# Kernel tuning notes

Hardware: AMD Instinct MI355X
Metric: run time of the kernel (lower is better)

Reference implementation:

```python
import jax, jax.numpy as jnp
import numpy as np

NF4 = jnp.array([-1.0, -0.6961928009986877, -0.5250730514526367, -0.39491748809814453,
                 -0.28444138169288635, -0.18477343022823334, -0.09105003625154495, 0.0,
                 0.07958029955625534, 0.16093020141124725, 0.24611230850219726,
                 0.33791524171829224, 0.44070982933044434, 0.5626170039176941,
                 0.7229568362236023, 1.0], dtype=jnp.float32)

OUT, IN = 8192, 8192
BLOCK = 64
NUMEL = OUT * IN


def setup_inputs() -> dict:
    key = jax.random.key(0)
    k1, k2, k3, k4 = jax.random.split(key, 4)
    x = jax.random.normal(k1, (64, IN), dtype=jnp.float32)
    packed = jax.random.randint(k2, (NUMEL // 2,), 0, 256, dtype=jnp.int32)
    absmax = jax.random.uniform(k3, (NUMEL // BLOCK,), dtype=jnp.float32)
    bias = jax.random.normal(k4, (OUT,), dtype=jnp.float32)
    return {"x": x, "packed": packed, "absmax": absmax, "bias": bias}


def nf4_dequantize(packed, absmax):
    # packed holds two 4-bit codes per byte: low nibble first, then high nibble
    low = packed & 15
    high = (packed >> 4) & 15
    q = jnp.stack([low, high], axis=1).reshape(-1)          # [numel]
    normalized = NF4[q]                                      # LUT dequant
    groups = normalized.reshape(-1, BLOCK)                   # [numel/block, block]
    w = (groups * absmax[:, None]).reshape(-1)[:NUMEL]
    return w.reshape(OUT, IN)


def reference(x, packed, absmax, bias):
    w = nf4_dequantize(packed, absmax)                       # [out, in]
    return jnp.dot(x, w.T) + bias                            # F.linear
```

## Files before the change

### kernel.cpp

```cpp
#include <hip/hip_runtime.h>
#include <hip/hip_bf16.h>

#define OUT_N 8192
#define IN_K  8192
#define M_ROWS 64

typedef __attribute__((ext_vector_type(8))) short  bf16x8;
typedef __attribute__((ext_vector_type(4))) float  f32x4;
typedef __attribute__((ext_vector_type(4))) int    int4v;

__device__ const float NF4_TAB[16] = {
  -1.0f, -0.6961928009986877f, -0.5250730514526367f, -0.39491748809814453f,
  -0.28444138169288635f, -0.18477343022823334f, -0.09105003625154495f, 0.0f,
  0.07958029955625534f, 0.16093020141124725f, 0.24611230850219726f,
  0.33791524171829224f, 0.44070982933044434f, 0.5626170039176941f,
  0.7229568362236023f, 1.0f };

static __device__ __forceinline__ unsigned short f2bf(float f) {
  union { __hip_bfloat16 h; unsigned short s; } u;
  u.h = __float2bfloat16(f);
  return u.s;
}

static __device__ __forceinline__ void gload_lds16(const void* g, void* s) {
  __builtin_amdgcn_global_load_lds((const __attribute__((address_space(1))) void*)g,
                                   (__attribute__((address_space(3))) void*)s,
                                   16, 0, 0);
}

__global__ __launch_bounds__(256) void qlin_prep(const float* __restrict__ x,
                                                 unsigned short* __restrict__ xf) {
  int t = blockIdx.x * 256 + threadIdx.x;
  int lane = t & 63, mt = (t >> 6) & 3, ks = t >> 8;
  int ri = lane & 15, kbb = lane >> 4;
  const float* src = x + (size_t)(mt * 16 + ri) * IN_K + ks * 32 + kbb * 8;
  f32x4 a = *(const f32x4*)src;
  f32x4 c = *(const f32x4*)(src + 4);
  bf16x8 o;
  o[0] = (short)f2bf(a[0]); o[1] = (short)f2bf(a[1]);
  o[2] = (short)f2bf(a[2]); o[3] = (short)f2bf(a[3]);
  o[4] = (short)f2bf(c[0]); o[5] = (short)f2bf(c[1]);
  o[6] = (short)f2bf(c[2]); o[7] = (short)f2bf(c[3]);
  ((bf16x8*)xf)[t] = o;
}

static __device__ __forceinline__ bf16x8 deq(const unsigned int* lut, int4v cur) {
  int4v bw;
  bw[0] = (int)lut[cur[0] & 255];
  bw[1] = (int)lut[cur[1] & 255];
  bw[2] = (int)lut[cur[2] & 255];
  bw[3] = (int)lut[cur[3] & 255];
  union { int4v i; bf16x8 h; } c; c.i = bw;
  return c.h;
}

#define STAGE(BUF, PH) {                                                      \
    const char* _s = xfb + (((size_t)(PH) * 4 + w) * 4096) + l * 16;          \
    gload_lds16(_s,        &ast[BUF][w][0]);                                  \
    gload_lds16(_s + 1024, &ast[BUF][w][64]);                                 \
    gload_lds16(_s + 2048, &ast[BUF][w][128]);                                \
    gload_lds16(_s + 3072, &ast[BUF][w][192]); }

#define CSTEP_BODY(S, PKV)                                                    \
    int _nk = KS + (S) + 4; if (_nk > NITm1) _nk = NITm1;                     \
    int4v _npk = *(const int4v*)(pcoal + (size_t)_nk * 64);                   \
    bf16x8 A0 = ast[cur][S][l];                                               \
    bf16x8 A1 = ast[cur][S][64 + l];                                          \
    bf16x8 A2 = ast[cur][S][128 + l];                                         \
    bf16x8 A3 = ast[cur][S][192 + l];                                         \
    int4v _c;                                                                 \
    _c[0] = __builtin_amdgcn_ds_bpermute(bpidx, PKV[0]);                      \
    _c[1] = __builtin_amdgcn_ds_bpermute(bpidx, PKV[1]);                      \
    _c[2] = __builtin_amdgcn_ds_bpermute(bpidx, PKV[2]);                      \
    _c[3] = __builtin_amdgcn_ds_bpermute(bpidx, PKV[3]);                      \
    bf16x8 b = deq(lut, _c);

#define CSTEP_EVEN(S, PKV) {                                                  \
    CSTEP_BODY(S, PKV)                                                        \
    sb0 = __builtin_amdgcn_mfma_f32_16x16x32_bf16(A0, b, zro, 0, 0, 0);       \
    sb1 = __builtin_amdgcn_mfma_f32_16x16x32_bf16(A1, b, zro, 0, 0, 0);       \
    sb2 = __builtin_amdgcn_mfma_f32_16x16x32_bf16(A2, b, zro, 0, 0, 0);       \
    sb3 = __builtin_amdgcn_mfma_f32_16x16x32_bf16(A3, b, zro, 0, 0, 0);       \
    PKV = _npk; }

#define CSTEP_ODD(S, PKV, AM) {                                               \
    CSTEP_BODY(S, PKV)                                                        \
    sb0 = __builtin_amdgcn_mfma_f32_16x16x32_bf16(A0, b, sb0, 0, 0, 0);       \
    sb1 = __builtin_amdgcn_mfma_f32_16x16x32_bf16(A1, b, sb1, 0, 0, 0);       \
    sb2 = __builtin_amdgcn_mfma_f32_16x16x32_bf16(A2, b, sb2, 0, 0, 0);       \
    sb3 = __builtin_amdgcn_mfma_f32_16x16x32_bf16(A3, b, sb3, 0, 0, 0);       \
    mn0 += sb0 * (AM); mn1 += sb1 * (AM);                                     \
    mn2 += sb2 * (AM); mn3 += sb3 * (AM);                                     \
    PKV = _npk; }

template<int NC>
__global__ __launch_bounds__(256, 4) void qlin_main(
    const int*   __restrict__ packed,
    const float* __restrict__ absmax,
    const unsigned short* __restrict__ xf,
    float*       __restrict__ parts) {
  constexpr int KCn   = IN_K / NC;
  constexpr int NIT   = KCn / 32;
  constexpr int NITm1 = NIT - 1;
  constexpr int NPH   = NIT / 4;
  constexpr int AMX   = NIT / 2 - 1;
  constexpr int LOG   = (NC == 8) ? 3 : 2;

  __shared__ unsigned int lut[256];
  __shared__ bf16x8 ast[2][4][256];
  {
    int t = threadIdx.x;
    unsigned lo = f2bf(NF4_TAB[t & 15]);
    unsigned hi = f2bf(NF4_TAB[(t >> 4) & 15]);
    lut[t] = lo | (hi << 16);
  }
  __syncthreads();

  const int l     = threadIdx.x & 63;
  const int w     = threadIdx.x >> 6;
  const int ntile = (int)blockIdx.x >> LOG;
  const int chunk = (int)blockIdx.x & (NC - 1);
  const int colg0 = ntile * 64 + w * 16;
  const int col   = colg0 + (l & 15);
  const int kb    = l >> 4;
  const int kc0   = chunk * KCn;
  const int ksg0  = kc0 >> 5;

  const char* pcoal = (const char*)packed
                    + ((size_t)(colg0 + (l >> 2)) * (IN_K / 2) + kc0 / 2) * 4
                    + (l & 3) * 16;
  const int bpidx = (((l & 15) << 2) | (l >> 4)) << 2;

  const char* xfb = (const char*)xf + (size_t)ksg0 * 4096;
  const float* aptr = absmax + (size_t)col * 128 + (kc0 >> 6);

  const f32x4 zro = {0.f, 0.f, 0.f, 0.f};
  f32x4 mn0 = zro, mn1 = zro, mn2 = zro, mn3 = zro;
  f32x4 sb0, sb1, sb2, sb3;
  int4v pk0, pk1, pk2, pk3;

  float amE = aptr[0], amO = aptr[1];
  STAGE(0, 0);
  __builtin_amdgcn_sched_barrier(0);
  pk0 = *(const int4v*)(pcoal);
  pk1 = *(const int4v*)(pcoal + 64);
  pk2 = *(const int4v*)(pcoal + 128);
  pk3 = *(const int4v*)(pcoal + 192);
  asm volatile("s_waitcnt vmcnt(4)" ::: "memory");
  __builtin_amdgcn_s_barrier();

  for (int ph = 0; ph < NPH; ++ph) {
    const int KS  = ph * 4;
    const int cur = ph & 1;

    int ia = 2 * ph + 2; if (ia > AMX) ia = AMX;
    int ib = 2 * ph + 3; if (ib > AMX) ib = AMX;
    float pmE = aptr[ia], pmO = aptr[ib];
    if (ph + 1 < NPH) STAGE(cur ^ 1, ph + 1);
    __builtin_amdgcn_sched_barrier(0);

    CSTEP_EVEN(0, pk0)
    CSTEP_ODD (1, pk1, amE)
    CSTEP_EVEN(2, pk2)
    CSTEP_ODD (3, pk3, amO)

    amE = pmE; amO = pmO;
    asm volatile("s_waitcnt vmcnt(4)" ::: "memory");
    asm volatile("s_waitcnt lgkmcnt(0)" ::: "memory");
    __builtin_amdgcn_s_barrier();
  }

  {
    float* tl = (float*)&ast[0][0][0];
    const int c  = w * 16 + (l & 15);
    const int r0 = kb * 4;
    tl[(0  + r0 + 0) * 68 + c] = mn0[0];
    tl[(0  + r0 + 1) * 68 + c] = mn0[1];
    tl[(0  + r0 + 2) * 68 + c] = mn0[2];
    tl[(0  + r0 + 3) * 68 + c] = mn0[3];
    tl[(16 + r0 + 0) * 68 + c] = mn1[0];
    tl[(16 + r0 + 1) * 68 + c] = mn1[1];
    tl[(16 + r0 + 2) * 68 + c] = mn1[2];
    tl[(16 + r0 + 3) * 68 + c] = mn1[3];
    tl[(32 + r0 + 0) * 68 + c] = mn2[0];
    tl[(32 + r0 + 1) * 68 + c] = mn2[1];
    tl[(32 + r0 + 2) * 68 + c] = mn2[2];
    tl[(32 + r0 + 3) * 68 + c] = mn2[3];
    tl[(48 + r0 + 0) * 68 + c] = mn3[0];
    tl[(48 + r0 + 1) * 68 + c] = mn3[1];
    tl[(48 + r0 + 2) * 68 + c] = mn3[2];
    tl[(48 + r0 + 3) * 68 + c] = mn3[3];
    __syncthreads();
    float* po = parts + (size_t)chunk * M_ROWS * OUT_N + (size_t)ntile * 64;
    const int t  = threadIdx.x;
    const int rr = t >> 4;
    const int cq = (t & 15) * 4;
    #pragma unroll
    for (int p = 0; p < 4; ++p) {
      const int row = p * 16 + rr;
      f32x4 v = *(const f32x4*)&tl[row * 68 + cq];
      *(f32x4*)(po + (size_t)row * OUT_N + cq) = v;
    }
  }
}

template<int NC>
__global__ __launch_bounds__(256) void qlin_reduce(
    const float* __restrict__ parts,
    const float* __restrict__ bias,
    float*       __restrict__ out) {
  const int TOT4 = M_ROWS * OUT_N / 4;
  int i4 = blockIdx.x * 256 + threadIdx.x;
  if (i4 >= TOT4) return;
  const f32x4* p = (const f32x4*)parts;
  f32x4 s = p[i4];
  #pragma unroll
  for (int c = 1; c < NC; ++c) s += p[i4 + c * TOT4];
  f32x4 bb = ((const f32x4*)bias)[i4 & (OUT_N / 4 - 1)];
  ((f32x4*)out)[i4] = s + bb;
}

extern "C" void kernel_launch(void* const* d_in, const int* in_sizes, int n_in,
                              void* d_out, int out_size, void* d_ws, size_t ws_size,
                              hipStream_t stream) {
  const float* x      = (const float*)d_in[0];
  const int*   packed = (const int*)d_in[1];
  const float* absmax = (const float*)d_in[2];
  const float* bias   = (const float*)d_in[3];
  float* out = (float*)d_out;

  unsigned short* xf = (unsigned short*)d_ws;
  float* parts = (float*)((char*)d_ws + (1 << 20));

  qlin_prep<<<(M_ROWS * IN_K / 8 + 255) / 256, 256, 0, stream>>>(x, xf);

  const size_t need8 = (size_t)(1 << 20)
                     + (size_t)8 * M_ROWS * OUT_N * sizeof(float);
  if (ws_size >= need8) {
    qlin_main<8><<<(OUT_N / 64) * 8, 256, 0, stream>>>(packed, absmax, xf, parts);
    qlin_reduce<8><<<(M_ROWS * OUT_N / 4 + 255) / 256, 256, 0, stream>>>(parts, bias, out);
  } else {
    qlin_main<4><<<(OUT_N / 64) * 4, 256, 0, stream>>>(packed, absmax, xf, parts);
    qlin_reduce<4><<<(M_ROWS * OUT_N / 4 + 255) / 256, 256, 0, stream>>>(parts, bias, out);
  }
}
```

Baseline: 41.61 us.

## Store split-K partials as bf16 tiles and pack bytes before a single bpermute

The split-K partial sums are now written as bf16 in a tile-contiguous layout, and the reduce kernel reads 8 bf16 per thread and accumulates in fp32. This halves partial-sum write and read traffic, at the cost of bf16 rounding error in each partial. Separately, the four packed bytes per step are combined into one 32-bit word, so one ds_bpermute is issued instead of four, which lowers cross-lane shuffle work in the inner loop. This assumes PKV elements hold values in 0..255, which holds when packed bytes are stored as int32.

After: 38.83 us, median of 2. -6.7%, faster.

```diff
diff --git a/kernel.cpp b/kernel.cpp
--- a/kernel.cpp
+++ b/kernel.cpp
@@ -8,6 +8,7 @@
 typedef __attribute__((ext_vector_type(8))) short  bf16x8;
 typedef __attribute__((ext_vector_type(4))) float  f32x4;
 typedef __attribute__((ext_vector_type(4))) int    int4v;
+typedef __attribute__((ext_vector_type(2))) int    int2v;
 
 __device__ const float NF4_TAB[16] = {
   -1.0f, -0.6961928009986877f, -0.5250730514526367f, -0.39491748809814453f,
@@ -44,12 +45,12 @@
   ((bf16x8*)xf)[t] = o;
 }
 
-static __device__ __forceinline__ bf16x8 deq(const unsigned int* lut, int4v cur) {
+static __device__ __forceinline__ bf16x8 deq(const unsigned int* lut, unsigned b) {
   int4v bw;
-  bw[0] = (int)lut[cur[0] & 255];
-  bw[1] = (int)lut[cur[1] & 255];
-  bw[2] = (int)lut[cur[2] & 255];
-  bw[3] = (int)lut[cur[3] & 255];
+  bw[0] = (int)lut[b & 255];
+  bw[1] = (int)lut[(b >> 8) & 255];
+  bw[2] = (int)lut[(b >> 16) & 255];
+  bw[3] = (int)lut[b >> 24];
   union { int4v i; bf16x8 h; } c; c.i = bw;
   return c.h;
 }
@@ -68,12 +69,10 @@
     bf16x8 A1 = ast[cur][S][64 + l];                                          \
     bf16x8 A2 = ast[cur][S][128 + l];                                         \
     bf16x8 A3 = ast[cur][S][192 + l];                                         \
-    int4v _c;                                                                 \
-    _c[0] = __builtin_amdgcn_ds_bpermute(bpidx, PKV[0]);                      \
-    _c[1] = __builtin_amdgcn_ds_bpermute(bpidx, PKV[1]);                      \
-    _c[2] = __builtin_amdgcn_ds_bpermute(bpidx, PKV[2]);                      \
-    _c[3] = __builtin_amdgcn_ds_bpermute(bpidx, PKV[3]);                      \
-    bf16x8 b = deq(lut, _c);
+    unsigned _pkd = (unsigned)PKV[0] | ((unsigned)PKV[1] << 8)                \
+                  | ((unsigned)PKV[2] << 16) | ((unsigned)PKV[3] << 24);      \
+    unsigned _bp = (unsigned)__builtin_amdgcn_ds_bpermute(bpidx, (int)_pkd);  \
+    bf16x8 b = deq(lut, _bp);
 
 #define CSTEP_EVEN(S, PKV) {                                                  \
     CSTEP_BODY(S, PKV)                                                        \
@@ -98,7 +97,7 @@
     const int*   __restrict__ packed,
     const float* __restrict__ absmax,
     const unsigned short* __restrict__ xf,
-    float*       __restrict__ parts) {
+    unsigned short* __restrict__ parts) {
   constexpr int KCn   = IN_K / NC;
   constexpr int NIT   = KCn / 32;
   constexpr int NITm1 = NIT - 1;
@@ -191,7 +190,7 @@
     tl[(48 + r0 + 2) * 68 + c] = mn3[2];
     tl[(48 + r0 + 3) * 68 + c] = mn3[3];
     __syncthreads();
-    float* po = parts + (size_t)chunk * M_ROWS * OUT_N + (size_t)ntile * 64;
+    unsigned short* po = parts + ((size_t)chunk * 128 + ntile) * 4096;
     const int t  = threadIdx.x;
     const int rr = t >> 4;
     const int cq = (t & 15) * 4;
@@ -199,25 +198,46 @@
     for (int p = 0; p < 4; ++p) {
       const int row = p * 16 + rr;
       f32x4 v = *(const f32x4*)&tl[row * 68 + cq];
-      *(f32x4*)(po + (size_t)row * OUT_N + cq) = v;
+      int2v o;
+      o[0] = (int)(f2bf(v[0]) | ((unsigned)f2bf(v[1]) << 16));
+      o[1] = (int)(f2bf(v[2]) | ((unsigned)f2bf(v[3]) << 16));
+      *(int2v*)(po + (size_t)row * 64 + cq) = o;
     }
   }
 }
 
 template<int NC>
 __global__ __launch_bounds__(256) void qlin_reduce(
-    const float* __restrict__ parts,
+    const unsigned short* __restrict__ parts,
     const float* __restrict__ bias,
     float*       __restrict__ out) {
-  const int TOT4 = M_ROWS * OUT_N / 4;
-  int i4 = blockIdx.x * 256 + threadIdx.x;
-  if (i4 >= TOT4) return;
-  const f32x4* p = (const f32x4*)parts;
-  f32x4 s = p[i4];
+  int e = blockIdx.x * 256 + threadIdx.x;
+  if (e >= M_ROWS * OUT_N / 8) return;
+  const int tile = e >> 9;
+  const int rem  = e & 511;
+  const int row  = rem >> 3;
+  const int oct  = rem & 7;
+  const size_t base = ((size_t)tile * 64 + row) * 64 + oct * 8;
+  constexpr size_t CS = (size_t)128 * 64 * 64;
+  float s[8] = {0,0,0,0,0,0,0,0};
   #pragma unroll
-  for (int c = 1; c < NC; ++c) s += p[i4 + c * TOT4];
-  f32x4 bb = ((const f32x4*)bias)[i4 & (OUT_N / 4 - 1)];
-  ((f32x4*)out)[i4] = s + bb;
+  for (int c = 0; c < NC; ++c) {
+    bf16x8 v = *(const bf16x8*)(parts + c * CS + base);
+    #pragma unroll
+    for (int j = 0; j < 8; ++j)
+      s[j] += __uint_as_float(((unsigned)(unsigned short)v[j]) << 16);
+  }
+  const int colb = tile * 64 + oct * 8;
+  const f32x4* bp = (const f32x4*)(bias + colb);
+  f32x4 b0 = bp[0], b1 = bp[1];
+  f32x4 o0, o1;
+  o0[0] = s[0] + b0[0]; o0[1] = s[1] + b0[1];
+  o0[2] = s[2] + b0[2]; o0[3] = s[3] + b0[3];
+  o1[0] = s[4] + b1[0]; o1[1] = s[5] + b1[1];
+  o1[2] = s[6] + b1[2]; o1[3] = s[7] + b1[3];
+  float* op = out + (size_t)row * OUT_N + colb;
+  *(f32x4*)op = o0;
+  *(f32x4*)(op + 4) = o1;
 }
 
 extern "C" void kernel_launch(void* const* d_in, const int* in_sizes, int n_in,
@@ -229,18 +249,18 @@
   const float* bias   = (const float*)d_in[3];
   float* out = (float*)d_out;
 
-  unsigned short* xf = (unsigned short*)d_ws;
-  float* parts = (float*)((char*)d_ws + (1 << 20));
+  unsigned short* xf    = (unsigned short*)d_ws;
+  unsigned short* parts = (unsigned short*)((char*)d_ws + (1 << 20));
 
   qlin_prep<<<(M_ROWS * IN_K / 8 + 255) / 256, 256, 0, stream>>>(x, xf);
 
-  const size_t need8 = (size_t)(1 << 20)
-                     + (size_t)8 * M_ROWS * OUT_N * sizeof(float);
+  const size_t chunk_bytes = (size_t)128 * 64 * 64 * sizeof(unsigned short);
+  const size_t need8 = (size_t)(1 << 20) + 8 * chunk_bytes;
   if (ws_size >= need8) {
-    qlin_main<8><<<(OUT_N / 64) * 8, 256, 0, stream>>>(packed, absmax, xf, parts);
-    qlin_reduce<8><<<(M_ROWS * OUT_N / 4 + 255) / 256, 256, 0, stream>>>(parts, bias, out);
+    qlin_main<8><<<128 * 8, 256, 0, stream>>>(packed, absmax, xf, parts);
+    qlin_reduce<8><<<(M_ROWS * OUT_N / 8 + 255) / 256, 256, 0, stream>>>(parts, bias, out);
   } else {
-    qlin_main<4><<<(OUT_N / 64) * 4, 256, 0, stream>>>(packed, absmax, xf, parts);
-    qlin_reduce<4><<<(M_ROWS * OUT_N / 4 + 255) / 256, 256, 0, stream>>>(parts, bias, out);
-  }
-}
+    qlin_main<4><<<128 * 4, 256, 0, stream>>>(packed, absmax, xf, parts);
+    qlin_reduce<4><<<(M_ROWS * OUT_N / 8 + 255) / 256, 256, 0, stream>>>(parts, bias, out);
+  }
+}
```
